# Kernel optimization log

Hardware: AMD Instinct MI355X
Metric: run time of the kernel (lower is better)

Reference implementation:

```python
import jax, jax.numpy as jnp
import numpy as np

B, T, C = 2, 2048, 1024
N_HEAD = 16
HEAD_DIM = C // N_HEAD


def setup_inputs() -> dict:
    key = jax.random.key(0)
    ks = jax.random.split(key, 5)
    s = 0.02
    return {
        "x": jax.random.normal(ks[0], (B, T, C), dtype=jnp.float32),
        "Wq": jax.random.normal(ks[1], (C, C), dtype=jnp.float32) * s,
        "bq": jnp.zeros((C,), dtype=jnp.float32),
        "Wk": jax.random.normal(ks[2], (C, C), dtype=jnp.float32) * s,
        "bk": jnp.zeros((C,), dtype=jnp.float32),
        "Wv": jax.random.normal(ks[3], (C, C), dtype=jnp.float32) * s,
        "bv": jnp.zeros((C,), dtype=jnp.float32),
        "Wo": jax.random.normal(ks[4], (C, C), dtype=jnp.float32) * s,
        "bo": jnp.zeros((C,), dtype=jnp.float32),
    }


def reference(x, Wq, bq, Wk, bk, Wv, bv, Wo, bo):
    b, t, c = x.shape
    h, d = N_HEAD, HEAD_DIM
    # projections -> [B, H, T, D]
    def proj(W, bias):
        return (x @ W.T + bias).reshape(b, t, h, d).transpose(0, 2, 1, 3)
    q = proj(Wq, bq)
    k = proj(Wk, bk)
    v = proj(Wv, bv)
    att = jnp.einsum("bhqd,bhkd->bhqk", q, k) / jnp.sqrt(jnp.float32(d))
    causal = jnp.tril(jnp.ones((t, t), dtype=bool))
    att = jnp.where(causal, att, jnp.float32(-jnp.inf))
    att = jax.nn.softmax(att, axis=-1)
    y = jnp.einsum("bhqk,bhkd->bhqd", att, v)  # [B,H,T,D]
    y = y.transpose(0, 2, 1, 3).reshape(b, t, c)
    return y @ Wo.T + bo
```

## Files before the change

### kernel.cpp

```cpp
#include <hip/hip_runtime.h>
#include <hip/hip_bf16.h>


namespace {

constexpr int TT = 2048;
constexpr int CC = 1024;
constexpr int HH = 16;
constexpr int DD = 64;

using bf16x8 = __attribute__((ext_vector_type(8))) __bf16;
using bf16x4 = __attribute__((ext_vector_type(4))) __bf16;
using f32x4  = __attribute__((ext_vector_type(4))) float;
using us8    = __attribute__((ext_vector_type(8))) unsigned short;

__device__ __forceinline__ unsigned short f2b(float f) {
  unsigned u = __float_as_uint(f);
  u += 0x7fffu + ((u >> 16) & 1u);
  return (unsigned short)(u >> 16);
}

__device__ __forceinline__ void gload16(const void* g, void* l) {
  __builtin_amdgcn_global_load_lds(
      (const __attribute__((address_space(1))) void*)g,
      (__attribute__((address_space(3))) void*)l, 16, 0, 0);
}

#if __has_builtin(__builtin_amdgcn_exp2f)
#define FEXP2 __builtin_amdgcn_exp2f
#else
#define FEXP2 exp2f
#endif

#define SCALE2 0.18033688011112042f

}

__global__ void k_cvt_all(const float* __restrict__ x,
                          const float* __restrict__ wq, const float* __restrict__ wk,
                          const float* __restrict__ wv, const float* __restrict__ wo,
                          unsigned short* __restrict__ dst) {
  const int i = blockIdx.x * 256 + threadIdx.x;
  const float* src; int off;
  if (i < 1048576)      { src = x;  off = i; }
  else if (i < 1310720) { src = wq; off = i - 1048576; }
  else if (i < 1572864) { src = wk; off = i - 1310720; }
  else if (i < 1835008) { src = wv; off = i - 1572864; }
  else                  { src = wo; off = i - 1835008; }
  float4 v = reinterpret_cast<const float4*>(src)[off];
  ushort4 o;
  o.x = f2b(v.x); o.y = f2b(v.y); o.z = f2b(v.z); o.w = f2b(v.w);
  reinterpret_cast<ushort4*>(dst)[i] = o;
}

__global__ __launch_bounds__(256, 3) void k_gemm_qkv(
    const unsigned short* __restrict__ A,
    const unsigned short* __restrict__ Wq,
    const unsigned short* __restrict__ Wk,
    const unsigned short* __restrict__ Wv,
    const float* __restrict__ bq,
    const float* __restrict__ bk,
    const float* __restrict__ bv,
    unsigned short* __restrict__ qd,
    unsigned short* __restrict__ kd,
    unsigned short* __restrict__ vd)
{
  __shared__ unsigned short la[2][128 * 32];
  __shared__ unsigned short lb[2][128 * 32];
  const int tid = threadIdx.x;
  const int lane = tid & 63;
  const int wid = tid >> 6;
  const int l15 = lane & 15, lg = lane >> 4;
  const int wm = (wid & 1) * 64, wn = (wid >> 1) * 64;
  const int bm = blockIdx.x;
  const int wsel = blockIdx.y >> 3;
  const int bnl = blockIdx.y & 7;

  const unsigned short* W = (wsel == 0) ? Wq : (wsel == 1) ? Wk : Wv;
  const float* bias = (wsel == 0) ? bq : (wsel == 1) ? bk : bv;

  const int srow = lane >> 2;
  const int sko  = (lane & 3) * 8;

  auto STAGE = [&](int buf, int kt) {
#pragma unroll
    for (int s = 0; s < 2; ++s) {
      const int seg = wid * 2 + s;
      const int row = seg * 16 + srow;
      gload16(&A[(bm * 128 + row) * CC + kt * 32 + sko], &la[buf][seg * 512]);
      gload16(&W[(bnl * 128 + row) * CC + kt * 32 + sko], &lb[buf][seg * 512]);
    }
  };

  f32x4 acc[4][4];
#pragma unroll
  for (int i = 0; i < 4; ++i)
#pragma unroll
    for (int j = 0; j < 4; ++j) acc[i][j] = f32x4{0.f, 0.f, 0.f, 0.f};

  STAGE(0, 0);
  asm volatile("s_waitcnt vmcnt(0)" ::: "memory");
  __syncthreads();

  int cur = 0;
  for (int kt = 0; kt < CC / 32; ++kt) {
    if (kt + 1 < CC / 32) STAGE(cur ^ 1, kt + 1);
    bf16x8 af[4], bf[4];
#pragma unroll
    for (int mi = 0; mi < 4; ++mi)
      af[mi] = __builtin_bit_cast(bf16x8,
        *reinterpret_cast<const us8*>(&la[cur][(wm + mi * 16 + l15) * 32 + lg * 8]));
#pragma unroll
    for (int ni = 0; ni < 4; ++ni)
      bf[ni] = __builtin_bit_cast(bf16x8,
        *reinterpret_cast<const us8*>(&lb[cur][(wn + ni * 16 + l15) * 32 + lg * 8]));
#pragma unroll
    for (int mi = 0; mi < 4; ++mi)
#pragma unroll
      for (int ni = 0; ni < 4; ++ni)
        acc[mi][ni] = __builtin_amdgcn_mfma_f32_16x16x32_bf16(af[mi], bf[ni], acc[mi][ni], 0, 0, 0);
    asm volatile("s_waitcnt vmcnt(0)" ::: "memory");
    __syncthreads();
    cur ^= 1;
  }

#pragma unroll
  for (int ni = 0; ni < 4; ++ni) {
    const int nl = bnl * 128 + wn + ni * 16 + l15;
    const float bvl = bias[nl];
    const int hh = nl >> 6, d = nl & (DD - 1);
#pragma unroll
    for (int mi = 0; mi < 4; ++mi) {
#pragma unroll
      for (int r = 0; r < 4; ++r) {
        const int m = bm * 128 + wm + mi * 16 + lg * 4 + r;
        const unsigned short bb = f2b(acc[mi][ni][r] + bvl);
        const int b = m >> 11, t = m & (TT - 1);
        if (wsel == 0)
          qd[((b * HH + hh) * TT + t) * DD + d] = bb;
        else if (wsel == 1)
          kd[((b * HH + hh) * TT + t) * DD + d] = bb;
        else
          vd[((b * HH + hh) * DD + d) * TT + t] = bb;
      }
    }
  }
}

__global__ __launch_bounds__(256, 2) void k_gemm_o(
    const unsigned short* __restrict__ A,
    const unsigned short* __restrict__ W,
    const float* __restrict__ bias,
    float* __restrict__ out)
{
  __shared__ unsigned short la[2][128 * 32];
  __shared__ unsigned short lb[2][64 * 32];
  const int tid = threadIdx.x;
  const int lane = tid & 63;
  const int wid = tid >> 6;
  const int l15 = lane & 15, lg = lane >> 4;
  const int wm = (wid & 1) * 64, wn = (wid >> 1) * 32;
  const int bm = blockIdx.x, bn = blockIdx.y;

  const int srow = lane >> 2;
  const int sko  = (lane & 3) * 8;

  auto STAGE = [&](int buf, int kt) {
#pragma unroll
    for (int s = 0; s < 2; ++s) {
      const int seg = wid * 2 + s;
      gload16(&A[(bm * 128 + seg * 16 + srow) * CC + kt * 32 + sko], &la[buf][seg * 512]);
    }
    gload16(&W[(bn * 64 + wid * 16 + srow) * CC + kt * 32 + sko], &lb[buf][wid * 512]);
  };

  f32x4 acc[4][2];
#pragma unroll
  for (int i = 0; i < 4; ++i)
#pragma unroll
    for (int j = 0; j < 2; ++j) acc[i][j] = f32x4{0.f, 0.f, 0.f, 0.f};

  STAGE(0, 0);
  asm volatile("s_waitcnt vmcnt(0)" ::: "memory");
  __syncthreads();

  int cur = 0;
  for (int kt = 0; kt < CC / 32; ++kt) {
    if (kt + 1 < CC / 32) STAGE(cur ^ 1, kt + 1);
    bf16x8 af[4], bf[2];
#pragma unroll
    for (int mi = 0; mi < 4; ++mi)
      af[mi] = __builtin_bit_cast(bf16x8,
        *reinterpret_cast<const us8*>(&la[cur][(wm + mi * 16 + l15) * 32 + lg * 8]));
#pragma unroll
    for (int ni = 0; ni < 2; ++ni)
      bf[ni] = __builtin_bit_cast(bf16x8,
        *reinterpret_cast<const us8*>(&lb[cur][(wn + ni * 16 + l15) * 32 + lg * 8]));
#pragma unroll
    for (int mi = 0; mi < 4; ++mi)
#pragma unroll
      for (int ni = 0; ni < 2; ++ni)
        acc[mi][ni] = __builtin_amdgcn_mfma_f32_16x16x32_bf16(af[mi], bf[ni], acc[mi][ni], 0, 0, 0);
    asm volatile("s_waitcnt vmcnt(0)" ::: "memory");
    __syncthreads();
    cur ^= 1;
  }

#pragma unroll
  for (int ni = 0; ni < 2; ++ni) {
    const int n = bn * 64 + wn + ni * 16 + l15;
    const float bvl = bias[n];
#pragma unroll
    for (int mi = 0; mi < 4; ++mi)
#pragma unroll
      for (int r = 0; r < 4; ++r) {
        const int m = bm * 128 + wm + mi * 16 + lg * 4 + r;
        out[m * CC + n] = acc[mi][ni][r] + bvl;
      }
  }
}

__global__ __launch_bounds__(64) void k_attn(
    const unsigned short* __restrict__ Q,
    const unsigned short* __restrict__ K,
    const unsigned short* __restrict__ VT,
    unsigned short* __restrict__ Y)
{
  __shared__ unsigned short pl[2][2][16][80];
  const int lane = threadIdx.x;
  const int l15 = lane & 15, lg = lane >> 4;
  const int bh = blockIdx.y;
  const int b = bh >> 4, h = bh & 15;
  const int p = blockIdx.x;
  const int qb0A = p * 32;
  const int qb0B = (63 - p) * 32;
  const int nktA = (qb0A + 95) >> 6;
  const int nktB = (qb0B + 95) >> 6;

  const unsigned short* Qh = Q + bh * TT * DD;
  const unsigned short* Kh = K + bh * TT * DD;
  const unsigned short* Vh = VT + bh * DD * TT;

  auto ldq = [&](bf16x8 (&qf)[2][2], int qb0) {
#pragma unroll
    for (int qi = 0; qi < 2; ++qi)
#pragma unroll
      for (int kk = 0; kk < 2; ++kk)
        qf[qi][kk] = __builtin_bit_cast(bf16x8,
          *reinterpret_cast<const us8*>(&Qh[(qb0 + qi * 16 + l15) * DD + kk * 32 + lg * 8]));
  };
  auto ldk = [&](bf16x8 (&kf)[4][2], int kb) {
#pragma unroll
    for (int f = 0; f < 4; ++f)
#pragma unroll
      for (int kk = 0; kk < 2; ++kk)
        kf[f][kk] = __builtin_bit_cast(bf16x8,
          *reinterpret_cast<const us8*>(&Kh[(kb + f * 16 + l15) * DD + kk * 32 + lg * 8]));
  };
  auto ldv = [&](bf16x8 (&vf)[2][4], int kb) {
#pragma unroll
    for (int kk = 0; kk < 2; ++kk)
#pragma unroll
      for (int dc = 0; dc < 4; ++dc)
        vf[kk][dc] = __builtin_bit_cast(bf16x8,
          *reinterpret_cast<const us8*>(&Vh[(dc * 16 + l15) * TT + kb + kk * 32 + lg * 8]));
  };

  bf16x8 qfA[2][2], qfB[2][2];
  ldq(qfA, qb0A); ldq(qfB, qb0B);

  f32x4 oA[2][4], oB[2][4];
  float mrA[2], lrA[2], mrB[2], lrB[2];
#pragma unroll
  for (int qi = 0; qi < 2; ++qi) {
    mrA[qi] = -INFINITY; lrA[qi] = 0.f;
    mrB[qi] = -INFINITY; lrB[qi] = 0.f;
#pragma unroll
    for (int dc = 0; dc < 4; ++dc) {
      oA[qi][dc] = f32x4{0.f, 0.f, 0.f, 0.f};
      oB[qi][dc] = f32x4{0.f, 0.f, 0.f, 0.f};
    }
  }

  auto processSet = [&](const int qb0, const bf16x8 (&qf)[2][2], f32x4 (&o)[2][4],
                        float (&mr)[2], float (&lr)[2],
                        unsigned short (&plS)[2][16][80],
                        const bf16x8 (&kf)[4][2], const bf16x8 (&vf)[2][4],
                        const int kbase) {
    f32x4 s[2][4];
#pragma unroll
    for (int qi = 0; qi < 2; ++qi)
#pragma unroll
      for (int f = 0; f < 4; ++f) {
        f32x4 t0 = __builtin_amdgcn_mfma_f32_16x16x32_bf16(kf[f][0], qf[qi][0],
                                                           f32x4{0.f,0.f,0.f,0.f}, 0, 0, 0);
        s[qi][f] = __builtin_amdgcn_mfma_f32_16x16x32_bf16(kf[f][1], qf[qi][1], t0, 0, 0, 0);
      }
    const bool needMask = (kbase + 63 > qb0);
#pragma unroll
    for (int qi = 0; qi < 2; ++qi) {
      const int qg = qb0 + qi * 16 + l15;
      float sv[4][4];
      float mt = -INFINITY;
#pragma unroll
      for (int f = 0; f < 4; ++f)
#pragma unroll
        for (int r = 0; r < 4; ++r) {
          float v = s[qi][f][r] * SCALE2;
          if (needMask) v = (kbase + f * 16 + lg * 4 + r <= qg) ? v : -INFINITY;
          sv[f][r] = v;
          mt = fmaxf(mt, v);
        }
      mt = fmaxf(mt, __shfl_xor(mt, 16));
      mt = fmaxf(mt, __shfl_xor(mt, 32));
      const float mn = fmaxf(mr[qi], mt);
      const float al = FEXP2(mr[qi] - mn);
      mr[qi] = mn;
      float rs = 0.f;
#pragma unroll
      for (int f = 0; f < 4; ++f) {
        const float p0 = FEXP2(sv[f][0] - mn), p1 = FEXP2(sv[f][1] - mn);
        const float p2 = FEXP2(sv[f][2] - mn), p3 = FEXP2(sv[f][3] - mn);
        rs += (p0 + p1) + (p2 + p3);
        bf16x4 pk;
        pk[0] = (__bf16)p0; pk[1] = (__bf16)p1; pk[2] = (__bf16)p2; pk[3] = (__bf16)p3;
        *reinterpret_cast<bf16x4*>(&plS[qi][l15][f * 16 + lg * 4]) = pk;
      }
      rs += __shfl_xor(rs, 16);
      rs += __shfl_xor(rs, 32);
      lr[qi] = lr[qi] * al + rs;
      float alr[4];
#pragma unroll
      for (int r = 0; r < 4; ++r) alr[r] = __shfl(al, lg * 4 + r);
#pragma unroll
      for (int dc = 0; dc < 4; ++dc)
#pragma unroll
        for (int r = 0; r < 4; ++r) o[qi][dc][r] *= alr[r];
    }
    asm volatile("s_waitcnt lgkmcnt(0)" ::: "memory");
    __builtin_amdgcn_sched_barrier(0);
#pragma unroll
    for (int qi = 0; qi < 2; ++qi) {
      const bf16x8 pa0 = __builtin_bit_cast(bf16x8,
        *reinterpret_cast<const us8*>(&plS[qi][l15][lg * 8]));
      const bf16x8 pa1 = __builtin_bit_cast(bf16x8,
        *reinterpret_cast<const us8*>(&plS[qi][l15][32 + lg * 8]));
#pragma unroll
      for (int dc = 0; dc < 4; ++dc) {
        o[qi][dc] = __builtin_amdgcn_mfma_f32_16x16x32_bf16(pa0, vf[0][dc], o[qi][dc], 0, 0, 0);
        o[qi][dc] = __builtin_amdgcn_mfma_f32_16x16x32_bf16(pa1, vf[1][dc], o[qi][dc], 0, 0, 0);
      }
    }
  };

  bf16x8 kf0[4][2], kf1[4][2];
  ldk(kf0, 0);
  for (int kt = 0; kt < nktB; kt += 2) {
    bf16x8 vf0[2][4];
    ldv(vf0, kt * 64);
    const int nx1 = (kt + 1 < nktB) ? kt + 1 : nktB - 1;
    ldk(kf1, nx1 * 64);
    processSet(qb0B, qfB, oB, mrB, lrB, pl[0], kf0, vf0, kt * 64);
    if (kt < nktA)
      processSet(qb0A, qfA, oA, mrA, lrA, pl[1], kf0, vf0, kt * 64);
    if (kt + 1 < nktB) {
      bf16x8 vf1[2][4];
      ldv(vf1, (kt + 1) * 64);
      const int nx2 = (kt + 2 < nktB) ? kt + 2 : nktB - 1;
      ldk(kf0, nx2 * 64);
      processSet(qb0B, qfB, oB, mrB, lrB, pl[0], kf1, vf1, (kt + 1) * 64);
      if (kt + 1 < nktA)
        processSet(qb0A, qfA, oA, mrA, lrA, pl[1], kf1, vf1, (kt + 1) * 64);
    }
  }

  auto epi = [&](int qb0, f32x4 (&o)[2][4], float (&lr)[2]) {
#pragma unroll
    for (int qi = 0; qi < 2; ++qi) {
      float linv[4];
#pragma unroll
      for (int r = 0; r < 4; ++r) linv[r] = 1.f / __shfl(lr[qi], lg * 4 + r);
#pragma unroll
      for (int r = 0; r < 4; ++r) {
        const int t = qb0 + qi * 16 + lg * 4 + r;
#pragma unroll
        for (int dc = 0; dc < 4; ++dc)
          Y[(b * TT + t) * CC + h * DD + dc * 16 + l15] = f2b(o[qi][dc][r] * linv[r]);
      }
    }
  };
  epi(qb0B, oB, lrB);
  epi(qb0A, oA, lrA);
}

extern "C" void kernel_launch(void* const* d_in, const int* in_sizes, int n_in,
                              void* d_out, int out_size, void* d_ws, size_t ws_size,
                              hipStream_t stream) {
  const float* x  = (const float*)d_in[0];
  const float* Wq = (const float*)d_in[1];
  const float* bq = (const float*)d_in[2];
  const float* Wk = (const float*)d_in[3];
  const float* bk = (const float*)d_in[4];
  const float* Wv = (const float*)d_in[5];
  const float* bv = (const float*)d_in[6];
  const float* Wo = (const float*)d_in[7];
  const float* bo = (const float*)d_in[8];
  float* out = (float*)d_out;

  unsigned short* ws  = (unsigned short*)d_ws;
  unsigned short* xb  = ws;
  unsigned short* wqb = xb  + 4194304;
  unsigned short* wkb = wqb + 1048576;
  unsigned short* wvb = wkb + 1048576;
  unsigned short* wob = wvb + 1048576;
  unsigned short* qb  = wob + 1048576;
  unsigned short* kb  = qb  + 4194304;
  unsigned short* vt  = kb  + 4194304;
  unsigned short* yb  = xb;

  k_cvt_all<<<8192, 256, 0, stream>>>(x, Wq, Wk, Wv, Wo, ws);

  k_gemm_qkv<<<dim3(32, 24), 256, 0, stream>>>(xb, wqb, wkb, wvb, bq, bk, bv, qb, kb, vt);

  k_attn<<<dim3(32, 32), 64, 0, stream>>>(qb, kb, vt, yb);

  k_gemm_o<<<dim3(32, 16), 256, 0, stream>>>(yb, wob, bo, out);
}
```

Measured before the change: 214.5 us.

## Keep two GEMM loads in flight with partial waitcnt and remap attention blocks

Both GEMM kernels now prefetch two k-tiles ahead using the two LDS buffers, wait with a partial vmcnt so the next tile's global-to-LDS loads stay outstanding during compute, and use raw s_barrier instead of __syncthreads. This aims to hide global load latency that the old per-iteration full vmcnt(0) wait exposed. Separately, the attention kernel remaps block indices with an XCD-style swizzle so blocks of the same head land on the same chiplet for better L2 reuse. The vmcnt counts depend on the exact number of loads each STAGE issues, so any miscount could cause races, and the swizzle assumes a 32x32 grid.

Measured after the change: 205.3 us. 1.04x faster.

```diff
diff --git a/kernel.cpp b/kernel.cpp
--- a/kernel.cpp
+++ b/kernel.cpp
@@ -98,31 +98,37 @@
 #pragma unroll
     for (int j = 0; j < 4; ++j) acc[i][j] = f32x4{0.f, 0.f, 0.f, 0.f};
 
-  STAGE(0, 0);
-  asm volatile("s_waitcnt vmcnt(0)" ::: "memory");
-  __syncthreads();
-
-  int cur = 0;
-  for (int kt = 0; kt < CC / 32; ++kt) {
-    if (kt + 1 < CC / 32) STAGE(cur ^ 1, kt + 1);
+  auto COMPUTE = [&](int buf) {
     bf16x8 af[4], bf[4];
 #pragma unroll
     for (int mi = 0; mi < 4; ++mi)
       af[mi] = __builtin_bit_cast(bf16x8,
-        *reinterpret_cast<const us8*>(&la[cur][(wm + mi * 16 + l15) * 32 + lg * 8]));
+        *reinterpret_cast<const us8*>(&la[buf][(wm + mi * 16 + l15) * 32 + lg * 8]));
 #pragma unroll
     for (int ni = 0; ni < 4; ++ni)
       bf[ni] = __builtin_bit_cast(bf16x8,
-        *reinterpret_cast<const us8*>(&lb[cur][(wn + ni * 16 + l15) * 32 + lg * 8]));
+        *reinterpret_cast<const us8*>(&lb[buf][(wn + ni * 16 + l15) * 32 + lg * 8]));
 #pragma unroll
     for (int mi = 0; mi < 4; ++mi)
 #pragma unroll
       for (int ni = 0; ni < 4; ++ni)
         acc[mi][ni] = __builtin_amdgcn_mfma_f32_16x16x32_bf16(af[mi], bf[ni], acc[mi][ni], 0, 0, 0);
-    asm volatile("s_waitcnt vmcnt(0)" ::: "memory");
-    __syncthreads();
+  };
+
+  STAGE(0, 0);
+  STAGE(1, 1);
+  int cur = 0;
+  for (int kt = 0; kt < CC / 32 - 1; ++kt) {
+    asm volatile("s_waitcnt vmcnt(4)" ::: "memory");
+    __builtin_amdgcn_s_barrier();
+    COMPUTE(cur);
+    __builtin_amdgcn_s_barrier();
+    if (kt < CC / 32 - 2) STAGE(cur, kt + 2);
     cur ^= 1;
   }
+  asm volatile("s_waitcnt vmcnt(0)" ::: "memory");
+  __builtin_amdgcn_s_barrier();
+  COMPUTE(cur);
 
 #pragma unroll
   for (int ni = 0; ni < 4; ++ni) {
@@ -180,31 +186,37 @@
 #pragma unroll
     for (int j = 0; j < 2; ++j) acc[i][j] = f32x4{0.f, 0.f, 0.f, 0.f};
 
-  STAGE(0, 0);
-  asm volatile("s_waitcnt vmcnt(0)" ::: "memory");
-  __syncthreads();
-
-  int cur = 0;
-  for (int kt = 0; kt < CC / 32; ++kt) {
-    if (kt + 1 < CC / 32) STAGE(cur ^ 1, kt + 1);
+  auto COMPUTE = [&](int buf) {
     bf16x8 af[4], bf[2];
 #pragma unroll
     for (int mi = 0; mi < 4; ++mi)
       af[mi] = __builtin_bit_cast(bf16x8,
-        *reinterpret_cast<const us8*>(&la[cur][(wm + mi * 16 + l15) * 32 + lg * 8]));
+        *reinterpret_cast<const us8*>(&la[buf][(wm + mi * 16 + l15) * 32 + lg * 8]));
 #pragma unroll
     for (int ni = 0; ni < 2; ++ni)
       bf[ni] = __builtin_bit_cast(bf16x8,
-        *reinterpret_cast<const us8*>(&lb[cur][(wn + ni * 16 + l15) * 32 + lg * 8]));
+        *reinterpret_cast<const us8*>(&lb[buf][(wn + ni * 16 + l15) * 32 + lg * 8]));
 #pragma unroll
     for (int mi = 0; mi < 4; ++mi)
 #pragma unroll
       for (int ni = 0; ni < 2; ++ni)
         acc[mi][ni] = __builtin_amdgcn_mfma_f32_16x16x32_bf16(af[mi], bf[ni], acc[mi][ni], 0, 0, 0);
-    asm volatile("s_waitcnt vmcnt(0)" ::: "memory");
-    __syncthreads();
+  };
+
+  STAGE(0, 0);
+  STAGE(1, 1);
+  int cur = 0;
+  for (int kt = 0; kt < CC / 32 - 1; ++kt) {
+    asm volatile("s_waitcnt vmcnt(3)" ::: "memory");
+    __builtin_amdgcn_s_barrier();
+    COMPUTE(cur);
+    __builtin_amdgcn_s_barrier();
+    if (kt < CC / 32 - 2) STAGE(cur, kt + 2);
     cur ^= 1;
   }
+  asm volatile("s_waitcnt vmcnt(0)" ::: "memory");
+  __builtin_amdgcn_s_barrier();
+  COMPUTE(cur);
 
 #pragma unroll
   for (int ni = 0; ni < 2; ++ni) {
@@ -229,9 +241,11 @@
   __shared__ unsigned short pl[2][2][16][80];
   const int lane = threadIdx.x;
   const int l15 = lane & 15, lg = lane >> 4;
-  const int bh = blockIdx.y;
+  const int wg = blockIdx.x + 32 * blockIdx.y;
+  const int swz = (wg & 7) * 128 + (wg >> 3);
+  const int p = swz & 31;
+  const int bh = swz >> 5;
   const int b = bh >> 4, h = bh & 15;
-  const int p = blockIdx.x;
   const int qb0A = p * 32;
   const int qb0B = (63 - p) * 32;
   const int nktA = (qb0A + 95) >> 6;
```
